# Kernel tuning notes

Hardware: AMD Instinct MI355X
Metric: run time of the kernel (lower is better)

The kernel has to match this reference:

```python
import jax, jax.numpy as jnp
import numpy as np

B, N, C, H, R = 16, 1024, 768, 12, 16
HD = C // H
SCALE = HD ** -0.5


def setup_inputs() -> dict:
    key = jax.random.key(0)
    ks = jax.random.split(key, 13)
    f = lambda k, shape, s=0.02: jax.random.normal(k, shape, dtype=jnp.float32) * s
    return {
        "x": jax.random.normal(ks[0], (B, N, C), dtype=jnp.float32),
        "W_qkv": f(ks[1], (3 * C, C)),
        "b_qkv": f(ks[2], (3 * C,)),
        "W_proj": f(ks[3], (C, C)),
        "b_proj": f(ks[4], (C,)),
        "A_q": f(ks[5], (R, C)),
        "B_q": f(ks[6], (C, R)),
        "A_k": f(ks[7], (R, C)),
        "B_k": f(ks[8], (C, R)),
        "A_v": f(ks[9], (R, C)),
        "B_v": f(ks[10], (C, R)),
        "A_o": f(ks[11], (R, C)),
        "B_o": f(ks[12], (C, R)),
    }


def _lora(x, A, Bu):
    # Adapter with no norm/act/bias, scaling=1.0: low-rank x @ A^T @ B^T
    return (x @ A.T) @ Bu.T


def _heads(t):
    # [B, N, C] -> [B, H, N, HD]
    return t.reshape(B, N, H, HD).transpose(0, 2, 1, 3)


def reference(x, W_qkv, b_qkv, W_proj, b_proj, A_q, B_q, A_k, B_k, A_v, B_v, A_o, B_o):
    qkv = x @ W_qkv.T + b_qkv                    # [B, N, 3C]
    qkv = qkv.reshape(B, N, 3, H, HD).transpose(2, 0, 3, 1, 4)  # [3, B, H, N, HD]
    q, k, v = qkv[0], qkv[1], qkv[2]
    q = q + _heads(_lora(x, A_q, B_q))
    k = k + _heads(_lora(x, A_k, B_k))
    v = v + _heads(_lora(x, A_v, B_v))
    attn = jnp.einsum("bhnd,bhmd->bhnm", q, k) * SCALE
    attn = jax.nn.softmax(attn, axis=-1)
    out = jnp.einsum("bhnm,bhmd->bhnd", attn, v)  # [B, H, N, HD]
    out = out.transpose(0, 2, 1, 3).reshape(B, N, C)
    out = out @ W_proj.T + b_proj
    out = out + _lora(out, A_o, B_o)
    return out
```

## Files before the change

### kernel.cpp

```cpp
#include <hip/hip_runtime.h>
#include <cmath>


#define DEVI __device__ __forceinline__

typedef float f32x4 __attribute__((ext_vector_type(4)));
typedef short s16x8 __attribute__((ext_vector_type(8)));
typedef __bf16 b16x8 __attribute__((ext_vector_type(8)));
typedef unsigned int u32x4 __attribute__((ext_vector_type(4)));

static constexpr int MTOT = 16384;
static constexpr int C = 768;
static constexpr int N3 = 2304;

DEVI unsigned short f2bf(float x) {
  unsigned int u = __builtin_bit_cast(unsigned int, x);
  return (unsigned short)((u + 0x7FFFu + ((u >> 16) & 1u)) >> 16);
}

DEVI f32x4 mfma16(s16x8 a, s16x8 b, f32x4 c) {
  return __builtin_amdgcn_mfma_f32_16x16x32_bf16(
      __builtin_bit_cast(b16x8, a), __builtin_bit_cast(b16x8, b), c, 0, 0, 0);
}

DEVI void async16(const void* g, void* l) {
  __builtin_amdgcn_global_load_lds(
      (__attribute__((address_space(1))) void*)g,
      (__attribute__((address_space(3))) void*)l, 16, 0, 0);
}


__global__ __launch_bounds__(256) void k_prep_x(const float* __restrict__ x,
                                                unsigned short* __restrict__ xb) {
  int idx = (blockIdx.x * 256 + threadIdx.x) * 4;
  float4 v = *(const float4*)(x + idx);
  uint2 p;
  p.x = (unsigned int)f2bf(v.x) | ((unsigned int)f2bf(v.y) << 16);
  p.y = (unsigned int)f2bf(v.z) | ((unsigned int)f2bf(v.w) << 16);
  *(uint2*)(xb + idx) = p;
}

__global__ __launch_bounds__(256) void k_prep_wqkv(
    const float* __restrict__ W, const float* __restrict__ Aq,
    const float* __restrict__ Bq, const float* __restrict__ Ak,
    const float* __restrict__ Bk, const float* __restrict__ Av,
    const float* __restrict__ Bv, unsigned short* __restrict__ out) {
  int idx = blockIdx.x * 256 + threadIdx.x;
  int n = idx / 768, c = idx - n * 768;
  int s = n / 768, co = n - s * 768;
  const float* A = (s == 0) ? Aq : (s == 1) ? Ak : Av;
  const float* Bm = (s == 0) ? Bq : (s == 1) ? Bk : Bv;
  float acc = W[idx];
#pragma unroll
  for (int r = 0; r < 16; ++r) acc += Bm[co * 16 + r] * A[r * 768 + c];
  out[idx] = f2bf(acc);
}

__global__ __launch_bounds__(256) void k_prep_M(const float* __restrict__ Ao,
                                                const float* __restrict__ Wp,
                                                float* __restrict__ M) {
  int r = blockIdx.x, t = threadIdx.x;
  float a0 = 0.f, a1 = 0.f, a2 = 0.f;
  for (int c = 0; c < 768; ++c) {
    float a = Ao[r * 768 + c];
    a0 += a * Wp[c * 768 + t];
    a1 += a * Wp[c * 768 + t + 256];
    a2 += a * Wp[c * 768 + t + 512];
  }
  M[r * 768 + t] = a0;
  M[r * 768 + t + 256] = a1;
  M[r * 768 + t + 512] = a2;
}

__global__ __launch_bounds__(256) void k_prep_wpe(const float* __restrict__ Wp,
                                                  const float* __restrict__ Bo,
                                                  const float* __restrict__ M,
                                                  unsigned short* __restrict__ out) {
  int idx = blockIdx.x * 256 + threadIdx.x;
  int n = idx / 768, j = idx - n * 768;
  float acc = Wp[idx];
#pragma unroll
  for (int r = 0; r < 16; ++r) acc += Bo[n * 16 + r] * M[r * 768 + j];
  out[idx] = f2bf(acc);
}

__global__ __launch_bounds__(256) void k_prep_beff(const float* __restrict__ bp,
                                                   const float* __restrict__ Ao,
                                                   const float* __restrict__ Bo,
                                                   float* __restrict__ beff) {
  __shared__ float bv[16];
  int t = threadIdx.x;
  if (t < 16) {
    float a0 = 0.f, a1 = 0.f, a2 = 0.f;
    for (int c = 0; c < 256; ++c) {
      a0 += Ao[t * 768 + c] * bp[c];
      a1 += Ao[t * 768 + c + 256] * bp[c + 256];
      a2 += Ao[t * 768 + c + 512] * bp[c + 512];
    }
    bv[t] = a0 + a1 + a2;
  }
  __syncthreads();
  int n = blockIdx.x * 256 + t;
  float acc = bp[n];
#pragma unroll
  for (int r = 0; r < 16; ++r) acc += Bo[n * 16 + r] * bv[r];
  beff[n] = acc;
}


template <bool SWAP>
__global__ __launch_bounds__(256) void k_gemm_qkv_t(
    const unsigned short* __restrict__ A, const unsigned short* __restrict__ Bw,
    const float* __restrict__ bias, int nblk0, unsigned short* __restrict__ qb,
    unsigned short* __restrict__ kb, unsigned short* __restrict__ vtb) {
  __shared__ short la[2][128 * 32];
  __shared__ short lb[2][128 * 32];
  const int t = threadIdx.x;
  const int w = t >> 6, l = t & 63;
  const int i = l & 15, qd = l >> 4;
  const int wm = w >> 1, wn = w & 1;
  const int mblk = blockIdx.x, nblk = nblk0 + blockIdx.y;

  const unsigned short* Ab = A + (size_t)(mblk * 128) * 768;
  const unsigned short* Bb = Bw + (size_t)(nblk * 128) * 768;
  const int sr = l >> 2;
  const int sc = (l & 3) * 8;

  auto stage = [&](int bufn, int kb_) {
    const int k0 = kb_ * 32;
#pragma unroll
    for (int j = 0; j < 2; ++j) {
      const int row = w * 32 + j * 16 + sr;
      async16(Ab + row * 768 + k0 + sc, &la[bufn][(w * 32 + j * 16) * 32]);
      async16(Bb + row * 768 + k0 + sc, &lb[bufn][(w * 32 + j * 16) * 32]);
    }
  };

  stage(0, 0);

  f32x4 acc[4][4] = {};

  for (int kb_ = 0; kb_ < 24; ++kb_) {
    const int buf = kb_ & 1;
    __syncthreads();
    if (kb_ < 23) stage(buf ^ 1, kb_ + 1);
    s16x8 af[4], bf[4];
#pragma unroll
    for (int mi = 0; mi < 4; ++mi)
      af[mi] = *(const s16x8*)&la[buf][(wm * 64 + mi * 16 + i) * 32 + qd * 8];
#pragma unroll
    for (int ni = 0; ni < 4; ++ni)
      bf[ni] = *(const s16x8*)&lb[buf][(wn * 64 + ni * 16 + i) * 32 + qd * 8];
#pragma unroll
    for (int mi = 0; mi < 4; ++mi)
#pragma unroll
      for (int ni = 0; ni < 4; ++ni) {
        if constexpr (SWAP)
          acc[mi][ni] = mfma16(bf[ni], af[mi], acc[mi][ni]);
        else
          acc[mi][ni] = mfma16(af[mi], bf[ni], acc[mi][ni]);
      }
  }

  const float c1 = 0.18033688011112042f;
  if constexpr (SWAP) {
#pragma unroll
    for (int ni = 0; ni < 4; ++ni) {
      const int n0 = nblk * 128 + wn * 64 + ni * 16 + qd * 4;
      const int s = n0 / 768;
      const int nrel = n0 - s * 768;
      const int h = nrel >> 6, d0 = nrel & 63;
      const float4 bv4 = *(const float4*)(bias + n0);
      unsigned short* dst = (s == 0) ? qb : kb;
      const float scl = (s == 0) ? c1 : 1.0f;
#pragma unroll
      for (int mi = 0; mi < 4; ++mi) {
        const int m = mblk * 128 + wm * 64 + mi * 16 + i;
        const int b = m >> 10, pos = m & 1023;
        uint2 pk;
        pk.x = (unsigned int)f2bf((acc[mi][ni][0] + bv4.x) * scl) |
               ((unsigned int)f2bf((acc[mi][ni][1] + bv4.y) * scl) << 16);
        pk.y = (unsigned int)f2bf((acc[mi][ni][2] + bv4.z) * scl) |
               ((unsigned int)f2bf((acc[mi][ni][3] + bv4.w) * scl) << 16);
        *(uint2*)&dst[(size_t)((b * 12 + h) * 1024 + pos) * 64 + d0] = pk;
      }
    }
  } else {
#pragma unroll
    for (int ni = 0; ni < 4; ++ni) {
      const int n = nblk * 128 + wn * 64 + ni * 16 + i;
      const int nrel = n - 1536;
      const int h = nrel >> 6, d = nrel & 63;
      const float bvv = bias[n];
#pragma unroll
      for (int mi = 0; mi < 4; ++mi) {
        const int m0 = mblk * 128 + wm * 64 + mi * 16 + qd * 4;
        const int b = m0 >> 10, pos0 = m0 & 1023;
        uint2 pk;
        pk.x = (unsigned int)f2bf(acc[mi][ni][0] + bvv) |
               ((unsigned int)f2bf(acc[mi][ni][1] + bvv) << 16);
        pk.y = (unsigned int)f2bf(acc[mi][ni][2] + bvv) |
               ((unsigned int)f2bf(acc[mi][ni][3] + bvv) << 16);
        *(uint2*)&vtb[(size_t)((b * 12 + h) * 64 + d) * 1024 + pos0] = pk;
      }
    }
  }
}


__global__ __launch_bounds__(256, 4) void k_attn(
    const unsigned short* __restrict__ qg, const unsigned short* __restrict__ kg,
    const unsigned short* __restrict__ vtg, unsigned short* __restrict__ og) {
  __shared__ short k_lds[2][64 * 64];
  __shared__ short vt_lds[2][64 * 64];

  const int t = threadIdx.x;
  const int w = t >> 6, l = t & 63;
  const int i = l & 15, qd = l >> 4;
  const int ix7 = l & 7;
  const int bh = blockIdx.x;
  const int qblk = blockIdx.y;
  const int h = bh % 12, b = bh / 12;

  const unsigned short* Qg = qg + (size_t)(bh * 1024 + qblk * 128) * 64;
  const unsigned short* Kg = kg + (size_t)bh * 1024 * 64;
  const unsigned short* Vtg = vtg + (size_t)bh * 64 * 1024;

  const int srl = l >> 3;
  const int sgc = (l & 7) ^ srl;

  s16x8 qf[2][2];
#pragma unroll
  for (int nq = 0; nq < 2; ++nq)
#pragma unroll
    for (int k0 = 0; k0 < 2; ++k0)
      qf[nq][k0] =
          *(const s16x8*)(Qg + (w * 32 + nq * 16 + i) * 64 + k0 * 32 + qd * 8);

  auto stage = [&](int bufn, int tkv) {
#pragma unroll
    for (int it = 0; it < 2; ++it) {
      const int rbase = it * 32 + w * 8;
      async16(Kg + (size_t)(tkv * 64 + rbase + srl) * 64 + sgc * 8,
              &k_lds[bufn][rbase * 64]);
      async16(Vtg + (size_t)(rbase + srl) * 1024 + tkv * 64 + sgc * 8,
              &vt_lds[bufn][rbase * 64]);
    }
  };

  stage(0, 0);

  f32x4 oacc[2][4] = {};
  f32x4 lacc[2] = {};
  const u32x4 ones_u = {0x3F803F80u, 0x3F803F80u, 0u, 0u};
  const s16x8 ones = __builtin_bit_cast(s16x8, ones_u);

  for (int tkv = 0; tkv < 16; ++tkv) {
    const int buf = tkv & 1;
    __syncthreads();
    if (tkv < 15) stage(buf ^ 1, tkv + 1);

#pragma unroll
    for (int mi = 0; mi < 4; ++mi) {
      f32x4 st[2] = {};
#pragma unroll
      for (int k0 = 0; k0 < 2; ++k0) {
        const s16x8 kf = *(const s16x8*)&k_lds[buf][(mi * 16 + i) * 64 +
                                                    (((k0 * 4 + qd) ^ ix7) * 8)];
        st[0] = mfma16(kf, qf[0][k0], st[0]);
        st[1] = mfma16(kf, qf[1][k0], st[1]);
      }

      s16x8 pa[2];
#pragma unroll
      for (int mq = 0; mq < 2; ++mq) {
        unsigned int u0 = __builtin_bit_cast(
            unsigned int, __builtin_amdgcn_exp2f(st[mq][0]));
        unsigned int u1 = __builtin_bit_cast(
            unsigned int, __builtin_amdgcn_exp2f(st[mq][1]));
        unsigned int u2 = __builtin_bit_cast(
            unsigned int, __builtin_amdgcn_exp2f(st[mq][2]));
        unsigned int u3 = __builtin_bit_cast(
            unsigned int, __builtin_amdgcn_exp2f(st[mq][3]));
        u32x4 p;
        p[0] = __builtin_amdgcn_perm(u1, u0, 0x07060302u);
        p[1] = __builtin_amdgcn_perm(u3, u2, 0x07060302u);
        p[2] = 0u;
        p[3] = 0u;
        pa[mq] = __builtin_bit_cast(s16x8, p);
      }

#pragma unroll
      for (int nd = 0; nd < 4; ++nd) {
        const uint2 v = *(const uint2*)&vt_lds[buf][(nd * 16 + i) * 64 +
                                                    ((((mi * 2 + (qd >> 1)) ^ ix7) * 8) +
                                                     (qd & 1) * 4)];
        u32x4 vu = {v.x, v.y, 0u, 0u};
        const s16x8 vf = __builtin_bit_cast(s16x8, vu);
        oacc[0][nd] = mfma16(pa[0], vf, oacc[0][nd]);
        oacc[1][nd] = mfma16(pa[1], vf, oacc[1][nd]);
      }
      lacc[0] = mfma16(pa[0], ones, lacc[0]);
      lacc[1] = mfma16(pa[1], ones, lacc[1]);
    }
  }

  const int orow0 = qblk * 128 + w * 32;
#pragma unroll
  for (int mq = 0; mq < 2; ++mq) {
    float linv[4];
#pragma unroll
    for (int r = 0; r < 4; ++r) linv[r] = 1.0f / lacc[mq][r];
#pragma unroll
    for (int nd = 0; nd < 4; ++nd)
#pragma unroll
      for (int r = 0; r < 4; ++r) {
        const int pos = orow0 + mq * 16 + qd * 4 + r;
        const int d = nd * 16 + i;
        og[(size_t)(b * 1024 + pos) * 768 + h * 64 + d] =
            f2bf(oacc[mq][nd][r] * linv[r]);
      }
  }
}


__global__ __launch_bounds__(256) void k_gemm_proj(
    const unsigned short* __restrict__ A, const unsigned short* __restrict__ Bw,
    const float* __restrict__ bias, float* __restrict__ out) {
  __shared__ short la[2][128 * 32];
  __shared__ short lb[2][128 * 32];
  const int t = threadIdx.x;
  const int w = t >> 6, l = t & 63;
  const int i = l & 15, qd = l >> 4;
  const int wm = w >> 1, wn = w & 1;
  const int mblk = blockIdx.x, nblk = blockIdx.y;

  const unsigned short* Ab = A + (size_t)(mblk * 128) * 768;
  const unsigned short* Bb = Bw + (size_t)(nblk * 128) * 768;
  const int sr = l >> 2;
  const int sc = (l & 3) * 8;

  auto stage = [&](int bufn, int kb_) {
    const int k0 = kb_ * 32;
#pragma unroll
    for (int j = 0; j < 2; ++j) {
      const int row = w * 32 + j * 16 + sr;
      async16(Ab + row * 768 + k0 + sc, &la[bufn][(w * 32 + j * 16) * 32]);
      async16(Bb + row * 768 + k0 + sc, &lb[bufn][(w * 32 + j * 16) * 32]);
    }
  };

  stage(0, 0);

  f32x4 acc[4][4] = {};

  for (int kb_ = 0; kb_ < 24; ++kb_) {
    const int buf = kb_ & 1;
    __syncthreads();
    if (kb_ < 23) stage(buf ^ 1, kb_ + 1);
    s16x8 af[4], bf[4];
#pragma unroll
    for (int mi = 0; mi < 4; ++mi)
      af[mi] = *(const s16x8*)&la[buf][(wm * 64 + mi * 16 + i) * 32 + qd * 8];
#pragma unroll
    for (int ni = 0; ni < 4; ++ni)
      bf[ni] = *(const s16x8*)&lb[buf][(wn * 64 + ni * 16 + i) * 32 + qd * 8];
#pragma unroll
    for (int mi = 0; mi < 4; ++mi)
#pragma unroll
      for (int ni = 0; ni < 4; ++ni)
        acc[mi][ni] = mfma16(bf[ni], af[mi], acc[mi][ni]);
  }

#pragma unroll
  for (int ni = 0; ni < 4; ++ni) {
    const int n0 = nblk * 128 + wn * 64 + ni * 16 + qd * 4;
    const float4 bv4 = *(const float4*)(bias + n0);
#pragma unroll
    for (int mi = 0; mi < 4; ++mi) {
      const int m = mblk * 128 + wm * 64 + mi * 16 + i;
      float4 o;
      o.x = acc[mi][ni][0] + bv4.x;
      o.y = acc[mi][ni][1] + bv4.y;
      o.z = acc[mi][ni][2] + bv4.z;
      o.w = acc[mi][ni][3] + bv4.w;
      *(float4*)&out[(size_t)m * 768 + n0] = o;
    }
  }
}


extern "C" void kernel_launch(void* const* d_in, const int* in_sizes, int n_in,
                              void* d_out, int out_size, void* d_ws, size_t ws_size,
                              hipStream_t stream) {
  const float* x = (const float*)d_in[0];
  const float* Wqkv = (const float*)d_in[1];
  const float* bqkv = (const float*)d_in[2];
  const float* Wp = (const float*)d_in[3];
  const float* bp = (const float*)d_in[4];
  const float* Aq = (const float*)d_in[5];
  const float* Bq = (const float*)d_in[6];
  const float* Ak = (const float*)d_in[7];
  const float* Bk = (const float*)d_in[8];
  const float* Av = (const float*)d_in[9];
  const float* Bv = (const float*)d_in[10];
  const float* Ao = (const float*)d_in[11];
  const float* Bo = (const float*)d_in[12];
  float* out = (float*)d_out;

  unsigned short* xb = (unsigned short*)d_ws;
  unsigned short* wqkvb = xb + (size_t)MTOT * C;
  unsigned short* wpeb = wqkvb + (size_t)N3 * C;
  unsigned short* qb = wpeb + (size_t)C * C;
  unsigned short* kb = qb + (size_t)MTOT * C;
  unsigned short* vtb = kb + (size_t)MTOT * C;
  float* Mbuf = (float*)(vtb + (size_t)MTOT * C);
  float* beff = Mbuf + 16 * 768;
  unsigned short* ob = xb;

  k_prep_x<<<12288, 256, 0, stream>>>(x, xb);
  k_prep_wqkv<<<6912, 256, 0, stream>>>(Wqkv, Aq, Bq, Ak, Bk, Av, Bv, wqkvb);
  k_prep_M<<<16, 256, 0, stream>>>(Ao, Wp, Mbuf);
  k_prep_wpe<<<2304, 256, 0, stream>>>(Wp, Bo, Mbuf, wpeb);
  k_prep_beff<<<3, 256, 0, stream>>>(bp, Ao, Bo, beff);

  k_gemm_qkv_t<true><<<dim3(128, 12), 256, 0, stream>>>(xb, wqkvb, bqkv, 0,
                                                        qb, kb, vtb);
  k_gemm_qkv_t<false><<<dim3(128, 6), 256, 0, stream>>>(xb, wqkvb, bqkv, 12,
                                                        qb, kb, vtb);
  k_attn<<<dim3(192, 8), 256, 0, stream>>>(qb, kb, vtb, ob);
  k_gemm_proj<<<dim3(128, 6), 256, 0, stream>>>(ob, wpeb, beff, out);
}
```

Measured before the change: 415.5 us.

## Use K=16 bf16 MFMA for PV in attention and parallelize prep reductions

In attention, the P·V and row-sum products previously ran through the 16x16x32 MFMA with the upper half of each operand zeroed. They now use the 16x16x16 bf16_1k MFMA when the compiler provides it, which avoids the wasted half of each instruction. The k_prep_M kernel is spread over a 16x12 grid with a four-way split reduction through LDS instead of 16 serial blocks. k_prep_beff now computes its 16 dot products cooperatively in one block instead of serially in 16 threads of each of 3 blocks. The risk is that the x16 MFMA may not be cheaper on this chip, or the builtin may be missing, in which case it falls back to the padded x32 form.

```diff
diff --git a/kernel.cpp b/kernel.cpp
--- a/kernel.cpp
+++ b/kernel.cpp
@@ -6,8 +6,10 @@
 
 typedef float f32x4 __attribute__((ext_vector_type(4)));
 typedef short s16x8 __attribute__((ext_vector_type(8)));
+typedef short s16x4 __attribute__((ext_vector_type(4)));
 typedef __bf16 b16x8 __attribute__((ext_vector_type(8)));
 typedef unsigned int u32x4 __attribute__((ext_vector_type(4)));
+typedef unsigned int u32x2 __attribute__((ext_vector_type(2)));
 
 static constexpr int MTOT = 16384;
 static constexpr int C = 768;
@@ -22,6 +24,20 @@
   return __builtin_amdgcn_mfma_f32_16x16x32_bf16(
       __builtin_bit_cast(b16x8, a), __builtin_bit_cast(b16x8, b), c, 0, 0, 0);
 }
+
+#if __has_builtin(__builtin_amdgcn_mfma_f32_16x16x16bf16_1k)
+#define HAVE_MFMA_X16 1
+DEVI f32x4 mfma16h(s16x4 a, s16x4 b, f32x4 c) {
+  return __builtin_amdgcn_mfma_f32_16x16x16bf16_1k(a, b, c, 0, 0, 0);
+}
+#else
+#define HAVE_MFMA_X16 0
+DEVI f32x4 mfma16h(s16x4 a, s16x4 b, f32x4 c) {
+  u32x2 au = __builtin_bit_cast(u32x2, a), bu = __builtin_bit_cast(u32x2, b);
+  u32x4 a8 = {au[0], au[1], 0u, 0u}, b8 = {bu[0], bu[1], 0u, 0u};
+  return mfma16(__builtin_bit_cast(s16x8, a8), __builtin_bit_cast(s16x8, b8), c);
+}
+#endif
 
 DEVI void async16(const void* g, void* l) {
   __builtin_amdgcn_global_load_lds(
@@ -59,17 +75,17 @@
 __global__ __launch_bounds__(256) void k_prep_M(const float* __restrict__ Ao,
                                                 const float* __restrict__ Wp,
                                                 float* __restrict__ M) {
-  int r = blockIdx.x, t = threadIdx.x;
-  float a0 = 0.f, a1 = 0.f, a2 = 0.f;
-  for (int c = 0; c < 768; ++c) {
-    float a = Ao[r * 768 + c];
-    a0 += a * Wp[c * 768 + t];
-    a1 += a * Wp[c * 768 + t + 256];
-    a2 += a * Wp[c * 768 + t + 512];
-  }
-  M[r * 768 + t] = a0;
-  M[r * 768 + t + 256] = a1;
-  M[r * 768 + t + 512] = a2;
+  __shared__ float red[4][64];
+  const int r = blockIdx.x, j0 = blockIdx.y * 64;
+  const int jl = threadIdx.x & 63, cs = threadIdx.x >> 6;
+  float acc = 0.f;
+#pragma unroll 4
+  for (int c = cs * 192; c < cs * 192 + 192; ++c)
+    acc += Ao[r * 768 + c] * Wp[c * 768 + j0 + jl];
+  red[cs][jl] = acc;
+  __syncthreads();
+  if (cs == 0)
+    M[r * 768 + j0 + jl] = red[0][jl] + red[1][jl] + red[2][jl] + red[3][jl];
 }
 
 __global__ __launch_bounds__(256) void k_prep_wpe(const float* __restrict__ Wp,
@@ -88,23 +104,30 @@
                                                    const float* __restrict__ Ao,
                                                    const float* __restrict__ Bo,
                                                    float* __restrict__ beff) {
+  __shared__ float red[256];
   __shared__ float bv[16];
-  int t = threadIdx.x;
-  if (t < 16) {
-    float a0 = 0.f, a1 = 0.f, a2 = 0.f;
-    for (int c = 0; c < 256; ++c) {
-      a0 += Ao[t * 768 + c] * bp[c];
-      a1 += Ao[t * 768 + c + 256] * bp[c + 256];
-      a2 += Ao[t * 768 + c + 512] * bp[c + 512];
-    }
-    bv[t] = a0 + a1 + a2;
-  }
+  const int t = threadIdx.x;
+  const int r = t >> 4, cs = t & 15;
+  float a = 0.f;
+#pragma unroll 4
+  for (int c = cs * 48; c < cs * 48 + 48; ++c) a += Ao[r * 768 + c] * bp[c];
+  red[t] = a;
   __syncthreads();
-  int n = blockIdx.x * 256 + t;
-  float acc = bp[n];
-#pragma unroll
-  for (int r = 0; r < 16; ++r) acc += Bo[n * 16 + r] * bv[r];
-  beff[n] = acc;
+  if (cs == 0) {
+    float s = 0.f;
+#pragma unroll
+    for (int k = 0; k < 16; ++k) s += red[r * 16 + k];
+    bv[r] = s;
+  }
+  __syncthreads();
+#pragma unroll
+  for (int it = 0; it < 3; ++it) {
+    const int n = it * 256 + t;
+    float acc = bp[n];
+#pragma unroll
+    for (int r2 = 0; r2 < 16; ++r2) acc += Bo[n * 16 + r2] * bv[r2];
+    beff[n] = acc;
+  }
 }
 
 
@@ -252,8 +275,8 @@
 
   f32x4 oacc[2][4] = {};
   f32x4 lacc[2] = {};
-  const u32x4 ones_u = {0x3F803F80u, 0x3F803F80u, 0u, 0u};
-  const s16x8 ones = __builtin_bit_cast(s16x8, ones_u);
+  const u32x2 ones_u = {0x3F803F80u, 0x3F803F80u};
+  const s16x4 ones4 = __builtin_bit_cast(s16x4, ones_u);
 
   for (int tkv = 0; tkv < 16; ++tkv) {
     const int buf = tkv & 1;
@@ -271,7 +294,7 @@
         st[1] = mfma16(kf, qf[1][k0], st[1]);
       }
 
-      s16x8 pa[2];
+      s16x4 pa4[2];
 #pragma unroll
       for (int mq = 0; mq < 2; ++mq) {
         unsigned int u0 = __builtin_bit_cast(
@@ -282,12 +305,10 @@
             unsigned int, __builtin_amdgcn_exp2f(st[mq][2]));
         unsigned int u3 = __builtin_bit_cast(
             unsigned int, __builtin_amdgcn_exp2f(st[mq][3]));
-        u32x4 p;
+        u32x2 p;
         p[0] = __builtin_amdgcn_perm(u1, u0, 0x07060302u);
         p[1] = __builtin_amdgcn_perm(u3, u2, 0x07060302u);
-        p[2] = 0u;
-        p[3] = 0u;
-        pa[mq] = __builtin_bit_cast(s16x8, p);
+        pa4[mq] = __builtin_bit_cast(s16x4, p);
       }
 
 #pragma unroll
@@ -295,13 +316,12 @@
         const uint2 v = *(const uint2*)&vt_lds[buf][(nd * 16 + i) * 64 +
                                                     ((((mi * 2 + (qd >> 1)) ^ ix7) * 8) +
                                                      (qd & 1) * 4)];
-        u32x4 vu = {v.x, v.y, 0u, 0u};
-        const s16x8 vf = __builtin_bit_cast(s16x8, vu);
-        oacc[0][nd] = mfma16(pa[0], vf, oacc[0][nd]);
-        oacc[1][nd] = mfma16(pa[1], vf, oacc[1][nd]);
-      }
-      lacc[0] = mfma16(pa[0], ones, lacc[0]);
-      lacc[1] = mfma16(pa[1], ones, lacc[1]);
+        const s16x4 vf = __builtin_bit_cast(s16x4, v);
+        oacc[0][nd] = mfma16h(pa4[0], vf, oacc[0][nd]);
+        oacc[1][nd] = mfma16h(pa4[1], vf, oacc[1][nd]);
+      }
+      lacc[0] = mfma16h(pa4[0], ones4, lacc[0]);
+      lacc[1] = mfma16h(pa4[1], ones4, lacc[1]);
     }
   }
 
@@ -420,9 +440,9 @@
 
   k_prep_x<<<12288, 256, 0, stream>>>(x, xb);
   k_prep_wqkv<<<6912, 256, 0, stream>>>(Wqkv, Aq, Bq, Ak, Bk, Av, Bv, wqkvb);
-  k_prep_M<<<16, 256, 0, stream>>>(Ao, Wp, Mbuf);
+  k_prep_M<<<dim3(16, 12), 256, 0, stream>>>(Ao, Wp, Mbuf);
   k_prep_wpe<<<2304, 256, 0, stream>>>(Wp, Bo, Mbuf, wpeb);
-  k_prep_beff<<<3, 256, 0, stream>>>(bp, Ao, Bo, beff);
+  k_prep_beff<<<1, 256, 0, stream>>>(bp, Ao, Bo, beff);
 
   k_gemm_qkv_t<true><<<dim3(128, 12), 256, 0, stream>>>(xb, wqkvb, bqkv, 0,
                                                         qb, kb, vtb);
```

New measurement: 344.7 us. -17.0%, faster.
